# Performance work log

Measured on AMD Instinct MI355X. Metric: run time of the kernel, lower is better.

## Reference

```python
import jax, jax.numpy as jnp
import numpy as np

LAMBDA_SPATIAL = 1.0  # fixed buffer, not trained
GAMMA_ADJ = 1.0       # fixed buffer, not trained


def setup_inputs() -> dict:
    key = jax.random.key(0)
    k1, k2, k3, k4 = jax.random.split(key, 4)
    B, T, N, D = 8, 20, 512, 64
    h = jax.random.normal(k1, (B, T, N, D), dtype=jnp.float32)
    velocities = jax.random.normal(k2, (B, T, N, 2), dtype=jnp.float32)
    adjacency_weighted = jax.random.uniform(k3, (B, T, N, N), dtype=jnp.float32)
    node_mask = jax.random.randint(k4, (B, T, N), 0, 2).astype(bool)
    return {
        "h": h,
        "velocities": velocities,
        "adjacency_weighted": adjacency_weighted,
        "node_mask": node_mask,
    }


def reference(h, velocities, adjacency_weighted, node_mask):
    # h: [B,T,N,d]; velocities: [B,T,N,2]; adjacency_weighted: [B,T,N,N]; node_mask: [B,T,N]
    mask = node_mask.astype(bool)
    pair_m = mask[..., :, None] & mask[..., None, :]          # [B,T,N,N]

    # pairwise squared velocity distance, Eq. (3)
    dv = velocities[..., :, None, :] - velocities[..., None, :, :]  # [B,T,N,N,2]
    d2 = jnp.maximum(jnp.sum(dv * dv, axis=-1), 0.0)                # [B,T,N,N]

    logits_s = -LAMBDA_SPATIAL * d2 + GAMMA_ADJ * adjacency_weighted
    neg = jnp.finfo(logits_s.dtype).min
    logits_s = jnp.where(pair_m, logits_s, neg)
    row_ok = mask[..., :, None]
    logits_s = jnp.where(row_ok, logits_s, jnp.zeros_like(logits_s))

    alpha = jax.nn.softmax(logits_s, axis=-1)
    alpha = jnp.nan_to_num(alpha, nan=0.0, posinf=0.0, neginf=0.0)
    alpha = alpha / jnp.maximum(jnp.sum(alpha, axis=-1, keepdims=True), 1e-8)
    h_spatial = jnp.matmul(alpha, h)                          # [B,T,N,d]

    # temporal path: masked mean-pool over nodes, T x T similarity softmax
    mask_f = mask.astype(h.dtype)
    denom = jnp.maximum(jnp.sum(mask_f, axis=-1, keepdims=True), 1.0)  # [B,T,1]
    h_mean = jnp.sum(h * mask_f[..., None], axis=-2) / denom           # [B,T,d]
    m_b = jnp.matmul(h_mean, jnp.swapaxes(h_mean, -1, -2))             # [B,T,T]
    beta = jax.nn.softmax(m_b, axis=-1)
    h_temporal = jnp.einsum("btu,bund->btnd", beta, h)                 # [B,T,N,d]

    out = (h + h_spatial + h_temporal) * mask_f[..., None]
    return out
```

## Files before the change

kernel.cpp:

```cpp
#include <hip/hip_runtime.h>
#include <float.h>

#define BB 8
#define TT 20
#define NN 512
#define DD 64
#define BT (BB*TT)

typedef __bf16 bf16x8 __attribute__((ext_vector_type(8)));
typedef float f32x4 __attribute__((ext_vector_type(4)));

__global__ __launch_bounds__(256) void kpre(const float* __restrict__ h,
                                            const float* __restrict__ vel,
                                            const int* __restrict__ mask,
                                            __bf16* __restrict__ ht,
                                            float* __restrict__ hpart,
                                            int* __restrict__ cpart,
                                            float4* __restrict__ colinfo,
                                            int* __restrict__ rows) {
    int bx = blockIdx.x;
    int bt = bx >> 3, slice = bx & 7;
    int n0 = slice * 64;
    int tid = threadIdx.x;
    const float* hp = h + ((size_t)bt * NN + n0) * DD;
    const int* mp = mask + (size_t)bt * NN + n0;
    short* htp = (short*)(ht + (size_t)bt * DD * NN) + n0;

    __shared__ __bf16 t[64][72];
    __shared__ float sred[16][64];

    int d4 = (tid & 15) << 2;
    int nl0 = tid >> 4;
    float s0 = 0.f, s1 = 0.f, s2 = 0.f, s3 = 0.f;
#pragma unroll
    for (int it = 0; it < 4; ++it) {
        int nl = it * 16 + nl0;
        float4 v = *(const float4*)(hp + (size_t)nl * DD + d4);
        if (mp[nl]) { s0 += v.x; s1 += v.y; s2 += v.z; s3 += v.w; }
        t[d4 + 0][nl] = (__bf16)v.x;
        t[d4 + 1][nl] = (__bf16)v.y;
        t[d4 + 2][nl] = (__bf16)v.z;
        t[d4 + 3][nl] = (__bf16)v.w;
    }
    int g = tid >> 4;
    sred[g][d4 + 0] = s0; sred[g][d4 + 1] = s1;
    sred[g][d4 + 2] = s2; sred[g][d4 + 3] = s3;
    __syncthreads();
#pragma unroll
    for (int it = 0; it < 4; ++it) {
        int idx = it * 256 + tid;
        int d = idx >> 4, s = idx & 15;
        short4 v4 = *(const short4*)&t[d][4 * s];
        *(short4*)(htp + (size_t)d * NN + 4 * s) = v4;
    }
    if (tid < 64) {
        float tot = 0.f;
#pragma unroll
        for (int k = 0; k < 16; ++k) tot += sred[k][tid];
        hpart[(size_t)bx * DD + tid] = tot;
    }
    if (tid < 64) {
        int j = n0 + tid;
        float2 v = ((const float2*)vel)[(size_t)bt * NN + j];
        int m = mp[tid];
        float cz = m ? -(v.x * v.x + v.y * v.y) : -3e38f;
        colinfo[(size_t)bt * NN + j] = make_float4(v.x, v.y, cz, 0.f);
        unsigned long long bal = __ballot(m != 0);
        int pos = __popcll(bal & ((1ull << tid) - 1ull));
        if (tid == 0) cpart[bx] = __popcll(bal);
        if (m) rows[(size_t)bt * NN + n0 + pos] = j;
    }
}

__global__ __launch_bounds__(256) void ktempbeta(const float* __restrict__ h,
                                                 const int* __restrict__ mask,
                                                 const float* __restrict__ hpart,
                                                 const int* __restrict__ cpart,
                                                 float* __restrict__ out) {
    int b = blockIdx.x >> 6;
    int q = (blockIdx.x & 63) * 256 + threadIdx.x;
    int n = q >> 5;
    int tid = threadIdx.x;
    __shared__ float hm[TT][DD];
    __shared__ float mbuf[TT][TT];
    __shared__ float cf[TT][TT];
    __shared__ float invc[TT];
    if (tid < TT) {
        int c = 0;
#pragma unroll
        for (int k = 0; k < 8; ++k) c += cpart[(b * TT + tid) * 8 + k];
        invc[tid] = 1.f / fmaxf((float)c, 1.f);
    }
    __syncthreads();
    for (int idx = tid; idx < TT * DD; idx += 256) {
        int t = idx >> 6, d = idx & 63;
        const float* pp = hpart + ((size_t)(b * TT + t) * 8) * DD + d;
        float s = 0.f;
#pragma unroll
        for (int k = 0; k < 8; ++k) s += pp[k * DD];
        hm[t][d] = s * invc[t];
    }
    __syncthreads();
    for (int p = tid; p < TT * TT; p += 256) {
        int t = p / TT, u = p % TT;
        float s = 0.f;
        for (int d = 0; d < DD; ++d) s += hm[t][d] * hm[u][d];
        mbuf[t][u] = s;
    }
    __syncthreads();
    if (tid < TT) {
        float mx = -FLT_MAX;
        for (int u = 0; u < TT; ++u) mx = fmaxf(mx, mbuf[tid][u]);
        float e[TT]; float sum = 0.f;
        for (int u = 0; u < TT; ++u) { e[u] = __expf(mbuf[tid][u] - mx); sum += e[u]; }
        float inv = 1.f / sum;
        for (int u = 0; u < TT; ++u)
            cf[tid][u] = e[u] * inv + (tid == u ? 1.f : 0.f);
    }
    __syncthreads();
    const float2* hp = (const float2*)h + (size_t)b * TT * 16384;
    float2* op = (float2*)out + (size_t)b * TT * 16384;
    const int* mp = mask + (size_t)b * TT * NN;
    float2 hv[TT];
#pragma unroll
    for (int u = 0; u < TT; ++u) hv[u] = hp[(size_t)u * 16384 + q];
    float2 z = {0.f, 0.f};
#pragma unroll
    for (int t = 0; t < TT; ++t) {
        float2 a = z;
#pragma unroll
        for (int u = 0; u < TT; ++u) {
            float c = cf[t][u];
            a.x += c * hv[u].x; a.y += c * hv[u].y;
        }
        int m = mp[(size_t)t * NN + n];
        op[(size_t)t * 16384 + q] = m ? a : z;
    }
}

__global__ __launch_bounds__(256) void kspatial(const float* __restrict__ adj,
                                                const float* __restrict__ vel,
                                                const int* __restrict__ cpart,
                                                const int* __restrict__ rows,
                                                const float4* __restrict__ colinfo,
                                                const __bf16* __restrict__ ht,
                                                float* __restrict__ out) {
    int bx = blockIdx.x;
    int x = bx & 7;
    int m8 = bx >> 3;
    int bt = x * 20 + (m8 >> 3);
    int i0 = (m8 & 7) * 64;

    const int* cp = cpart + bt * 8;
    int cs[8];
#pragma unroll
    for (int s = 0; s < 8; ++s) cs[s] = cp[s];
    int n_act = 0;
#pragma unroll
    for (int s = 0; s < 8; ++s) n_act += cs[s];
    if (i0 >= n_act) return;

    int tid = threadIdx.x;
    int w = tid >> 6, lane = tid & 63;
    int arow = lane & 15;
    int kg = lane >> 4;

    __shared__ __bf16 hs[64][520];
    __shared__ float4 ci[NN];

    for (int idx = tid; idx < NN; idx += 256)
        ci[idx] = colinfo[(size_t)bt * NN + idx];

    const ushort* htb = (const ushort*)(ht + (size_t)bt * DD * NN);
#pragma unroll
    for (int it = 0; it < 16; ++it) {
        int chunk = it * 256 + tid;
        int r = chunk >> 6;
        int cc = chunk & 63;
        *(uint4*)(&hs[r][cc * 8]) = *(const uint4*)(htb + (size_t)r * NN + cc * 8);
    }

    int slot = i0 + w * 16 + arow;
    int slotc = slot < n_act ? slot : n_act - 1;
    int row = 0, base = 0;
#pragma unroll
    for (int s = 0; s < 8; ++s) {
        if (slotc >= base && slotc < base + cs[s])
            row = rows[(size_t)bt * NN + s * 64 + (slotc - base)];
        base += cs[s];
    }
    float2 rv = ((const float2*)vel)[(size_t)bt * NN + row];
    float vx2 = 2.f * rv.x, vy2 = 2.f * rv.y;

    const float* arowp = adj + ((size_t)bt * NN + row) * NN;

    f32x4 zero = {0.f, 0.f, 0.f, 0.f};
    f32x4 acc[4];
#pragma unroll
    for (int nt = 0; nt < 4; ++nt) acc[nt] = zero;
    float lsum = 0.f;
    __syncthreads();

    f32x4 a01[16], a23[16];
    {
        const f32x4* p0 = (const f32x4*)(arowp + kg * 8);
        a01[0] = __builtin_nontemporal_load(p0);
        a23[0] = __builtin_nontemporal_load(p0 + 1);
        a01[1] = __builtin_nontemporal_load(p0 + 8);
        a23[1] = __builtin_nontemporal_load(p0 + 9);
    }
#pragma unroll
    for (int c = 0; c < 16; ++c) {
        if (c < 14) {
            const f32x4* pn = (const f32x4*)(arowp + kg * 8 + (c + 2) * 32);
            a01[c + 2] = __builtin_nontemporal_load(pn);
            a23[c + 2] = __builtin_nontemporal_load(pn + 1);
        }
        int jb = kg * 8 + c * 32;
        const float4* ccp = &ci[jb];
        float p[8];
#pragma unroll
        for (int e = 0; e < 8; ++e) {
            float av = (e < 4) ? a01[c][e] : a23[c][e - 4];
            float4 cc = ccp[e];
            float l = av + cc.z + vx2 * cc.x + vy2 * cc.y;
            p[e] = __expf(l);
        }
        lsum += ((p[0] + p[1]) + (p[2] + p[3])) + ((p[4] + p[5]) + (p[6] + p[7]));
        bf16x8 af;
#pragma unroll
        for (int e = 0; e < 8; ++e) af[e] = (__bf16)p[e];
#pragma unroll
        for (int nt = 0; nt < 4; ++nt) {
            bf16x8 bf = *(const bf16x8*)(&hs[nt * 16 + arow][jb]);
            acc[nt] = __builtin_amdgcn_mfma_f32_16x16x32_bf16(af, bf, acc[nt], 0, 0, 0);
        }
    }

    lsum += __shfl_xor(lsum, 16, 64);
    lsum += __shfl_xor(lsum, 32, 64);
    float inv = 1.0f / fmaxf(lsum, 1e-8f);

    float* op = out + (size_t)bt * NN * DD;
#pragma unroll
    for (int q = 0; q < 4; ++q) {
        int cr = kg * 4 + q;
        int s2 = i0 + w * 16 + cr;
        int r2 = __shfl(row, cr, 64);
        float iv = __shfl(inv, cr, 64);
        if (s2 < n_act) {
#pragma unroll
            for (int nt = 0; nt < 4; ++nt) {
                size_t o = (size_t)r2 * DD + nt * 16 + arow;
                op[o] = op[o] + acc[nt][q] * iv;
            }
        }
    }
}

extern "C" void kernel_launch(void* const* d_in, const int* in_sizes, int n_in,
                              void* d_out, int out_size, void* d_ws, size_t ws_size,
                              hipStream_t stream) {
    const float* h   = (const float*)d_in[0];
    const float* vel = (const float*)d_in[1];
    const float* adj = (const float*)d_in[2];
    const int* mask  = (const int*)d_in[3];
    float* out = (float*)d_out;

    char* ws = (char*)d_ws;
    __bf16* ht      = (__bf16*)ws;                       ws += (size_t)BT * DD * NN * 2;
    float4* colinfo = (float4*)ws;                       ws += (size_t)BT * NN * 16;
    float* hpart    = (float*)ws;                        ws += (size_t)BT * 8 * DD * 4;
    int* cpart      = (int*)ws;                          ws += (size_t)BT * 8 * 4;
    int* rows       = (int*)ws;

    kpre<<<BT * 8, 256, 0, stream>>>(h, vel, mask, ht, hpart, cpart, colinfo, rows);
    ktempbeta<<<BB * 64, 256, 0, stream>>>(h, mask, hpart, cpart, out);
    kspatial<<<BT * 8, 256, 0, stream>>>(adj, vel, cpart, rows, colinfo, ht, out);
}
```

Before: 64.97 us.

## Read bf16 copy of h in temporal kernel and drop nontemporal adjacency loads

The pre-pass now also writes a row-major bf16 copy of h. The temporal kernel reads that copy instead of fp32 h, handles four elements per thread, and launches half as many blocks. The spatial kernel's adjacency loads switch from nontemporal builtins to plain loads. The aim is to halve the temporal kernel's h read traffic, at the cost of an extra bf16 write in the pre-pass and bf16 rounding of h in the identity and temporal terms.

```diff
diff --git a/kernel.cpp b/kernel.cpp
--- a/kernel.cpp
+++ b/kernel.cpp
@@ -8,12 +8,14 @@
 #define BT (BB*TT)
 
 typedef __bf16 bf16x8 __attribute__((ext_vector_type(8)));
+typedef __bf16 bf16x4 __attribute__((ext_vector_type(4)));
 typedef float f32x4 __attribute__((ext_vector_type(4)));
 
 __global__ __launch_bounds__(256) void kpre(const float* __restrict__ h,
                                             const float* __restrict__ vel,
                                             const int* __restrict__ mask,
                                             __bf16* __restrict__ ht,
+                                            __bf16* __restrict__ hb16,
                                             float* __restrict__ hpart,
                                             int* __restrict__ cpart,
                                             float4* __restrict__ colinfo,
@@ -37,10 +39,13 @@
         int nl = it * 16 + nl0;
         float4 v = *(const float4*)(hp + (size_t)nl * DD + d4);
         if (mp[nl]) { s0 += v.x; s1 += v.y; s2 += v.z; s3 += v.w; }
-        t[d4 + 0][nl] = (__bf16)v.x;
-        t[d4 + 1][nl] = (__bf16)v.y;
-        t[d4 + 2][nl] = (__bf16)v.z;
-        t[d4 + 3][nl] = (__bf16)v.w;
+        __bf16 b0 = (__bf16)v.x, b1 = (__bf16)v.y, b2 = (__bf16)v.z, b3 = (__bf16)v.w;
+        t[d4 + 0][nl] = b0;
+        t[d4 + 1][nl] = b1;
+        t[d4 + 2][nl] = b2;
+        t[d4 + 3][nl] = b3;
+        bf16x4 pv = {b0, b1, b2, b3};
+        *(bf16x4*)(hb16 + ((size_t)bt * NN + n0 + nl) * DD + d4) = pv;
     }
     int g = tid >> 4;
     sred[g][d4 + 0] = s0; sred[g][d4 + 1] = s1;
@@ -72,14 +77,14 @@
     }
 }
 
-__global__ __launch_bounds__(256) void ktempbeta(const float* __restrict__ h,
+__global__ __launch_bounds__(256) void ktempbeta(const __bf16* __restrict__ hb16,
                                                  const int* __restrict__ mask,
                                                  const float* __restrict__ hpart,
                                                  const int* __restrict__ cpart,
                                                  float* __restrict__ out) {
-    int b = blockIdx.x >> 6;
-    int q = (blockIdx.x & 63) * 256 + threadIdx.x;
-    int n = q >> 5;
+    int b = blockIdx.x >> 5;
+    int q4 = (blockIdx.x & 31) * 256 + threadIdx.x;
+    int n = q4 >> 4;
     int tid = threadIdx.x;
     __shared__ float hm[TT][DD];
     __shared__ float mbuf[TT][TT];
@@ -118,23 +123,28 @@
             cf[tid][u] = e[u] * inv + (tid == u ? 1.f : 0.f);
     }
     __syncthreads();
-    const float2* hp = (const float2*)h + (size_t)b * TT * 16384;
-    float2* op = (float2*)out + (size_t)b * TT * 16384;
+    const bf16x4* hp = (const bf16x4*)hb16 + (size_t)b * TT * 8192;
+    float4* op = (float4*)out + (size_t)b * TT * 8192;
     const int* mp = mask + (size_t)b * TT * NN;
-    float2 hv[TT];
-#pragma unroll
-    for (int u = 0; u < TT; ++u) hv[u] = hp[(size_t)u * 16384 + q];
-    float2 z = {0.f, 0.f};
+    float4 hv[TT];
+#pragma unroll
+    for (int u = 0; u < TT; ++u) {
+        bf16x4 x = hp[(size_t)u * 8192 + q4];
+        hv[u].x = (float)x[0]; hv[u].y = (float)x[1];
+        hv[u].z = (float)x[2]; hv[u].w = (float)x[3];
+    }
+    float4 z = {0.f, 0.f, 0.f, 0.f};
 #pragma unroll
     for (int t = 0; t < TT; ++t) {
-        float2 a = z;
+        float4 a = z;
 #pragma unroll
         for (int u = 0; u < TT; ++u) {
             float c = cf[t][u];
             a.x += c * hv[u].x; a.y += c * hv[u].y;
+            a.z += c * hv[u].z; a.w += c * hv[u].w;
         }
         int m = mp[(size_t)t * NN + n];
-        op[(size_t)t * 16384 + q] = m ? a : z;
+        op[(size_t)t * 8192 + q4] = m ? a : z;
     }
 }
 
@@ -204,17 +214,17 @@
     f32x4 a01[16], a23[16];
     {
         const f32x4* p0 = (const f32x4*)(arowp + kg * 8);
-        a01[0] = __builtin_nontemporal_load(p0);
-        a23[0] = __builtin_nontemporal_load(p0 + 1);
-        a01[1] = __builtin_nontemporal_load(p0 + 8);
-        a23[1] = __builtin_nontemporal_load(p0 + 9);
+        a01[0] = p0[0];
+        a23[0] = p0[1];
+        a01[1] = p0[8];
+        a23[1] = p0[9];
     }
 #pragma unroll
     for (int c = 0; c < 16; ++c) {
         if (c < 14) {
             const f32x4* pn = (const f32x4*)(arowp + kg * 8 + (c + 2) * 32);
-            a01[c + 2] = __builtin_nontemporal_load(pn);
-            a23[c + 2] = __builtin_nontemporal_load(pn + 1);
+            a01[c + 2] = pn[0];
+            a23[c + 2] = pn[1];
         }
         int jb = kg * 8 + c * 32;
         const float4* ccp = &ci[jb];
@@ -269,12 +279,13 @@
 
     char* ws = (char*)d_ws;
     __bf16* ht      = (__bf16*)ws;                       ws += (size_t)BT * DD * NN * 2;
+    __bf16* hb16    = (__bf16*)ws;                       ws += (size_t)BT * NN * DD * 2;
     float4* colinfo = (float4*)ws;                       ws += (size_t)BT * NN * 16;
     float* hpart    = (float*)ws;                        ws += (size_t)BT * 8 * DD * 4;
     int* cpart      = (int*)ws;                          ws += (size_t)BT * 8 * 4;
     int* rows       = (int*)ws;
 
-    kpre<<<BT * 8, 256, 0, stream>>>(h, vel, mask, ht, hpart, cpart, colinfo, rows);
-    ktempbeta<<<BB * 64, 256, 0, stream>>>(h, mask, hpart, cpart, out);
+    kpre<<<BT * 8, 256, 0, stream>>>(h, vel, mask, ht, hb16, hpart, cpart, colinfo, rows);
+    ktempbeta<<<BB * 32, 256, 0, stream>>>(hb16, mask, hpart, cpart, out);
     kspatial<<<BT * 8, 256, 0, stream>>>(adj, vel, cpart, rows, colinfo, ht, out);
 }
```

New measurement: 63.19 us. 2.7% less time.
